# Performance work log

Measured on AMD Instinct MI355X. Metric: run time of the kernel, lower is better.

## Reference

```python
import math
import jax, jax.numpy as jnp
import numpy as np

B, N, D, H, HID = 2, 2048, 1024, 16, 4096
KS = (7, 25, 49)

def _alibi_slopes(n):
    def p2(m):
        start = 2.0 ** (-(2.0 ** (-(math.log2(m) - 3))))
        return [start * (start ** i) for i in range(m)]
    if math.log2(n).is_integer():
        s = p2(n)
    else:
        cp2 = 2 ** int(math.floor(math.log2(n)))
        s = p2(cp2) + p2(2 * cp2)[0::2][: n - cp2]
    return jnp.asarray(s, dtype=jnp.float32)

def _ln(x, g, b, eps=1e-5):
    m = x.mean(-1, keepdims=True)
    v = ((x - m) ** 2).mean(-1, keepdims=True)
    return (x - m) / jnp.sqrt(v + eps) * g + b

def _dwconv(x, w, pl, pr, mode, bias=None):
    # x: (B, D, L) channels-first, w: (D, 1, k) depthwise kernel
    xp = jnp.pad(x, ((0, 0), (0, 0), (pl, pr)), mode=mode)
    y = jax.lax.conv_general_dilated(xp, w, (1,), 'VALID',
                                     dimension_numbers=('NCH', 'OIH', 'NCH'),
                                     feature_group_count=x.shape[1])
    if bias is not None:
        y = y + bias[None, :, None]
    return y

def _forward(x, periodic_bias, alpha, dw7, dw25, dw49, ln1_g, ln1_b, ln2_g, ln2_b,
             Wq, bq, Wk, bk, Wv, bv, Wo, bo, W1, b1, W2, b2, tw, tb):
    Bx, Nx, Dm = x.shape
    hd = Dm // H
    # --- series decomposition: softmax-weighted multi-scale moving averages ---
    xt = x.transpose(0, 2, 1)  # (B, D, N)
    branches = [_dwconv(xt, w, k // 2, k // 2, 'reflect')
                for w, k in ((dw7, 7), (dw25, 25), (dw49, 49))]
    wmix = jax.nn.softmax(alpha)
    T = sum(br * wi for br, wi in zip(branches, wmix)).transpose(0, 2, 1)  # trend (B,N,D)
    S = x - T  # seasonal
    # --- ALiBi self-attention on normalized seasonal part ---
    sn = _ln(S, ln1_g, ln1_b)
    q = (jnp.einsum('bnd,ed->bne', sn, Wq) + bq).reshape(Bx, Nx, H, hd)
    k = (jnp.einsum('bnd,ed->bne', sn, Wk) + bk).reshape(Bx, Nx, H, hd)
    v = (jnp.einsum('bnd,ed->bne', sn, Wv) + bv).reshape(Bx, Nx, H, hd)
    logits = jnp.einsum('bqhd,bkhd->bhqk', q, k) / np.float32(np.sqrt(hd))
    idx = jnp.arange(Nx)
    dist = jnp.maximum(idx[None, :] - idx[:, None], 0).astype(jnp.float32)  # clamp(j-i, 0)
    slopes = _alibi_slopes(H)
    logits = logits - slopes[None, :, None, None] * dist[None, None] + periodic_bias[None, None]
    attn = jax.nn.softmax(logits, axis=-1)
    o = jnp.einsum('bhqk,bkhd->bqhd', attn, v).reshape(Bx, Nx, Dm)
    y = jnp.einsum('bnd,ed->bne', o, Wo) + bo
    x_s = S + y
    # --- dense FFN (exact GELU, as torch nn.GELU default) ---
    h = _ln(x_s, ln2_g, ln2_b)
    ffn = jnp.einsum('bnh,dh->bnd',
                     jax.nn.gelu(jnp.einsum('bnd,hd->bnh', h, W1) + b1, approximate=False),
                     W2) + b2
    x_s = x_s + ffn
    # --- trend path: depthwise conv k=5, zero padding 2 ---
    t_out = _dwconv(T.transpose(0, 2, 1), tw, 2, 2, 'constant', tb).transpose(0, 2, 1)
    return x_s + t_out

def setup_inputs():
    key = jax.random.key(0)
    ks = jax.random.split(key, 12)
    def lin(k, o, i):
        return jax.random.normal(k, (o, i), jnp.float32) / np.float32(np.sqrt(i))
    return {
        'x': jax.random.normal(ks[0], (B, N, D), jnp.float32),
        'periodic_bias': 0.1 * jax.random.normal(ks[1], (N, N), jnp.float32),
        'alpha': jnp.zeros((len(KS),), jnp.float32),
        'dw7': jnp.full((D, 1, 7), 1.0 / 7, jnp.float32),
        'dw25': jnp.full((D, 1, 25), 1.0 / 25, jnp.float32),
        'dw49': jnp.full((D, 1, 49), 1.0 / 49, jnp.float32),
        'ln1_g': jnp.ones((D,), jnp.float32), 'ln1_b': jnp.zeros((D,), jnp.float32),
        'ln2_g': jnp.ones((D,), jnp.float32), 'ln2_b': jnp.zeros((D,), jnp.float32),
        'Wq': lin(ks[2], D, D), 'bq': jnp.zeros((D,), jnp.float32),
        'Wk': lin(ks[3], D, D), 'bk': jnp.zeros((D,), jnp.float32),
        'Wv': lin(ks[4], D, D), 'bv': jnp.zeros((D,), jnp.float32),
        'Wo': lin(ks[5], D, D), 'bo': jnp.zeros((D,), jnp.float32),
        'W1': lin(ks[6], HID, D), 'b1': jnp.zeros((HID,), jnp.float32),
        'W2': lin(ks[7], D, HID), 'b2': jnp.zeros((D,), jnp.float32),
        'tw': 0.1 * jax.random.normal(ks[8], (D, 1, 5), jnp.float32),
        'tb': jnp.zeros((D,), jnp.float32),
    }

def reference(x, periodic_bias, alpha, dw7, dw25, dw49, ln1_g, ln1_b, ln2_g, ln2_b,
              Wq, bq, Wk, bk, Wv, bv, Wo, bo, W1, b1, W2, b2, tw, tb):
    out = _forward(x, periodic_bias, alpha, dw7, dw25, dw49, ln1_g, ln1_b, ln2_g, ln2_b,
                   Wq, bq, Wk, bk, Wv, bv, Wo, bo, W1, b1, W2, b2, tw, tb)
    return (out, jnp.zeros((), out.dtype))
```

## Files before the change

kernel.cpp:

```cpp
#include <hip/hip_runtime.h>
#include <cstdint>

#define BB 2
#define NN 2048
#define DD 1024
#define HH 16
#define HD 64
#define HID_ 4096
#define MM (BB*NN)

typedef __bf16 bf16x8 __attribute__((ext_vector_type(8)));
typedef float  f32x4  __attribute__((ext_vector_type(4)));

__device__ inline void gload_lds16(const void* g, void* l) {
  __builtin_amdgcn_global_load_lds((const __attribute__((address_space(1))) char*)g,
                                   (__attribute__((address_space(3))) char*)l, 16, 0, 0);
}

__global__ void k_wcomb(const float* __restrict__ alpha, const float* __restrict__ dw7,
                        const float* __restrict__ dw25, const float* __restrict__ dw49,
                        float* __restrict__ wc) {
  int t = blockIdx.x;
  float a0 = alpha[0], a1 = alpha[1], a2 = alpha[2];
  float mx = fmaxf(a0, fmaxf(a1, a2));
  float e0 = __expf(a0 - mx), e1 = __expf(a1 - mx), e2 = __expf(a2 - mx);
  float inv = 1.f / (e0 + e1 + e2);
  float w0 = e0 * inv, w1 = e1 * inv, w2 = e2 * inv;
  for (int d = threadIdx.x; d < DD; d += blockDim.x) {
    float v = w2 * dw49[d * 49 + t];
    if (t >= 12 && t <= 36) v += w1 * dw25[d * 25 + (t - 12)];
    if (t >= 21 && t <= 27) v += w0 * dw7[d * 7 + (t - 21)];
    wc[t * DD + d] = v;
  }
}

__global__ void k_bias3(const float* __restrict__ bq, const float* __restrict__ bk,
                        const float* __restrict__ bv, float* __restrict__ b3) {
  for (int i = threadIdx.x; i < 3 * DD; i += blockDim.x) {
    const float* s = (i < DD) ? bq : (i < 2 * DD ? bk : bv);
    b3[i] = s[i & (DD - 1)];
  }
}

__global__ __launch_bounds__(256) void k_cvtall(const float* __restrict__ Wq, const float* __restrict__ Wk,
                         const float* __restrict__ Wv, const float* __restrict__ Wo,
                         const float* __restrict__ W1, const float* __restrict__ W2,
                         __bf16* __restrict__ dst) {
  size_t i = ((size_t)blockIdx.x * 256 + threadIdx.x) * 4;
  const float* s;
  if (i < 1048576u) s = Wq + i;
  else if (i < 2097152u) s = Wk + (i - 1048576u);
  else if (i < 3145728u) s = Wv + (i - 2097152u);
  else if (i < 4194304u) s = Wo + (i - 3145728u);
  else if (i < 8388608u) s = W1 + (i - 4194304u);
  else s = W2 + (i - 8388608u);
  float4 v = *(const float4*)s;
  dst[i] = (__bf16)v.x; dst[i+1] = (__bf16)v.y; dst[i+2] = (__bf16)v.z; dst[i+3] = (__bf16)v.w;
}

__global__ __launch_bounds__(256) void k_pbt(const float* __restrict__ pb,
                                             __bf16* __restrict__ pbt) {
  int q = blockIdx.x;
  int qt16 = q >> 4, qm = q & 15;
  for (int k = threadIdx.x; k < NN; k += 256) {
    float v = pb[(size_t)q * NN + k] * 1.4426950408889634f;
    int kt = k >> 4, g = (k >> 2) & 3, rr = k & 3;
    pbt[((size_t)qt16 * 128 + kt) * 256 + (qm + 16 * g) * 4 + rr] = (__bf16)v;
  }
}

__global__ __launch_bounds__(256) void k_decomp(const float* __restrict__ x,
                                                const float* __restrict__ wc,
                                                float* __restrict__ T, float* __restrict__ S) {
  int bid = blockIdx.x;
  int db = bid & 3, ns = (bid >> 2) & 127, b = bid >> 9;
  int d = db * 256 + threadIdx.x;
  const float* xb = x + (size_t)b * NN * DD + d;
  float xw[64];
#pragma unroll
  for (int i = 0; i < 64; ++i) {
    int n = ns * 16 - 24 + i;
    n = (n < 0) ? -n : n;
    n = (n > NN - 1) ? 2 * (NN - 1) - n : n;
    xw[i] = xb[(size_t)n * DD];
  }
  float acc[16];
#pragma unroll
  for (int i = 0; i < 16; ++i) acc[i] = 0.f;
#pragma unroll
  for (int t = 0; t < 49; ++t) {
    float wv = wc[t * DD + d];
#pragma unroll
    for (int i = 0; i < 16; ++i) acc[i] = fmaf(wv, xw[i + t], acc[i]);
  }
  size_t base = ((size_t)b * NN + ns * 16) * DD + d;
#pragma unroll
  for (int i = 0; i < 16; ++i) {
    T[base + (size_t)i * DD] = acc[i];
    S[base + (size_t)i * DD] = xw[i + 24] - acc[i];
  }
}

__global__ __launch_bounds__(256) void k_tout(const float* __restrict__ T,
                                              const float* __restrict__ tw,
                                              const float* __restrict__ tb,
                                              float* __restrict__ tout) {
  int bid = blockIdx.x;
  int db = bid & 3, ns = (bid >> 2) & 127, b = bid >> 9;
  int d = db * 256 + threadIdx.x;
  const float* Tb = T + (size_t)b * NN * DD + d;
  float xw[20];
#pragma unroll
  for (int i = 0; i < 20; ++i) {
    int n = ns * 16 - 2 + i;
    xw[i] = (n < 0 || n >= NN) ? 0.f : Tb[(size_t)n * DD];
  }
  float bv = tb[d];
  float acc[16];
#pragma unroll
  for (int i = 0; i < 16; ++i) acc[i] = bv;
#pragma unroll
  for (int t = 0; t < 5; ++t) {
    float wv = tw[d * 5 + t];
#pragma unroll
    for (int i = 0; i < 16; ++i) acc[i] = fmaf(wv, xw[i + t], acc[i]);
  }
  size_t base = ((size_t)b * NN + ns * 16) * DD + d;
#pragma unroll
  for (int i = 0; i < 16; ++i) tout[base + (size_t)i * DD] = acc[i];
}

__global__ __launch_bounds__(256) void k_ln(const float* __restrict__ x,
                                            const float* __restrict__ g,
                                            const float* __restrict__ bt,
                                            __bf16* __restrict__ y) {
  int row = blockIdx.x;
  const float* xr = x + (size_t)row * DD;
  int i = threadIdx.x * 4;
  float4 v = *(const float4*)&xr[i];
  float s = v.x + v.y + v.z + v.w;
  float sq = v.x * v.x + v.y * v.y + v.z * v.z + v.w * v.w;
#pragma unroll
  for (int m = 1; m <= 32; m <<= 1) { s += __shfl_xor(s, m); sq += __shfl_xor(sq, m); }
  __shared__ float rs[4], rq[4];
  int wid = threadIdx.x >> 6;
  if ((threadIdx.x & 63) == 0) { rs[wid] = s; rq[wid] = sq; }
  __syncthreads();
  s = rs[0] + rs[1] + rs[2] + rs[3];
  sq = rq[0] + rq[1] + rq[2] + rq[3];
  float mean = s * (1.f / DD);
  float var = sq * (1.f / DD) - mean * mean;
  float rstd = rsqrtf(var + 1e-5f);
  float4 gv = *(const float4*)&g[i];
  float4 bv = *(const float4*)&bt[i];
  __bf16* yr = y + (size_t)row * DD + i;
  yr[0] = (__bf16)((v.x - mean) * rstd * gv.x + bv.x);
  yr[1] = (__bf16)((v.y - mean) * rstd * gv.y + bv.y);
  yr[2] = (__bf16)((v.z - mean) * rstd * gv.z + bv.z);
  yr[3] = (__bf16)((v.w - mean) * rstd * gv.w + bv.w);
}

template <int EPI, int BNT>
__global__ __launch_bounds__(256) void k_gemm(const __bf16* __restrict__ A,
                                              const __bf16* __restrict__ Bw, int K,
                                              const float* __restrict__ bias,
                                              const float* __restrict__ aux1,
                                              const float* __restrict__ aux2,
                                              float* __restrict__ outf,
                                              __bf16* __restrict__ outb) {
  constexpr int NFR = BNT / 32;
  __shared__ __bf16 aS[2][128 * 32];
  __shared__ __bf16 bS[2][BNT * 32];
  const int tid = threadIdx.x;
  const int lane = tid & 63;
  const int wid = tid >> 6;
  const int wm = wid >> 1, wn = wid & 1;
  const int r = lane & 15, gq = lane >> 4;
  const int m0 = blockIdx.y * 128;
  const int n0 = blockIdx.x * BNT;

  f32x4 acc[4][NFR];
#pragma unroll
  for (int mi = 0; mi < 4; ++mi)
#pragma unroll
    for (int ni = 0; ni < NFR; ++ni) acc[mi][ni] = (f32x4){0.f, 0.f, 0.f, 0.f};

  auto stage = [&](int bufi, int k0) {
#pragma unroll
    for (int i = 0; i < 2; ++i) {
      int e = i * 2048 + tid * 8;
      int row = e >> 5, col = e & 31;
      gload_lds16(A + (size_t)(m0 + row) * K + k0 + col, &aS[bufi][e]);
    }
#pragma unroll
    for (int i = 0; i < BNT / 64; ++i) {
      int e = i * 2048 + tid * 8;
      int row = e >> 5, col = e & 31;
      gload_lds16(Bw + (size_t)(n0 + row) * K + k0 + col, &bS[bufi][e]);
    }
  };

  stage(0, 0);
  const int nk = K >> 5;
  int buf = 0;
  for (int kt = 0; kt < nk; ++kt) {
    __syncthreads();
    if (kt + 1 < nk) stage(buf ^ 1, (kt + 1) << 5);
    bf16x8 af[4], bfr[NFR];
#pragma unroll
    for (int mi = 0; mi < 4; ++mi)
      af[mi] = *reinterpret_cast<const bf16x8*>(&aS[buf][(wm * 64 + mi * 16 + r) * 32 + gq * 8]);
#pragma unroll
    for (int ni = 0; ni < NFR; ++ni)
      bfr[ni] = *reinterpret_cast<const bf16x8*>(&bS[buf][(wn * (BNT / 2) + ni * 16 + r) * 32 + gq * 8]);
#pragma unroll
    for (int mi = 0; mi < 4; ++mi)
#pragma unroll
      for (int ni = 0; ni < NFR; ++ni)
        acc[mi][ni] = __builtin_amdgcn_mfma_f32_16x16x32_bf16(af[mi], bfr[ni], acc[mi][ni], 0, 0, 0);
    buf ^= 1;
  }

#pragma unroll
  for (int mi = 0; mi < 4; ++mi) {
#pragma unroll
    for (int ni = 0; ni < NFR; ++ni) {
      int colg = n0 + wn * (BNT / 2) + ni * 16 + r;
      float bcol = bias[colg];
#pragma unroll
      for (int rr = 0; rr < 4; ++rr) {
        int mg = m0 + wm * 64 + mi * 16 + gq * 4 + rr;
        float val = acc[mi][ni][rr] + bcol;
        if constexpr (EPI == 0) {
          int which = colg >> 10, e = colg & 1023;
          int hh = e >> 6, d = e & 63;
          int b = mg >> 11, nq = mg & (NN - 1);
          if (which == 2) {
            int nl = nq & 63, kk = nl & 31;
            int slot = ((kk >> 4) << 2) | (((kk >> 2) & 3) << 3) | (kk & 3) | (nl & 32);
            int nqp = (nq & ~63) | slot;
            outb[(size_t)2 * (BB * HH * NN * HD) +
                 ((size_t)((b * HH + hh) * HD + d)) * NN + nqp] = (__bf16)val;
          } else {
            outb[(size_t)which * (BB * HH * NN * HD) +
                 ((size_t)(b * HH + hh) * NN + nq) * HD + d] = (__bf16)val;
          }
        } else if constexpr (EPI == 1) {
          size_t idx = (size_t)mg * DD + colg;
          outf[idx] = aux1[idx] + val;
        } else if constexpr (EPI == 2) {
          float gl = val * 0.5f * (1.f + erff(val * 0.70710678118f));
          outb[(size_t)mg * HID_ + colg] = (__bf16)gl;
        } else {
          size_t idx = (size_t)mg * DD + colg;
          outf[idx] = val + aux1[idx] + aux2[idx];
        }
      }
    }
  }
}

__global__ __launch_bounds__(512) void k_attn(const __bf16* __restrict__ qb,
                                              const __bf16* __restrict__ kb,
                                              const __bf16* __restrict__ vtb,
                                              const __bf16* __restrict__ pbt,
                                              __bf16* __restrict__ ob) {
  __shared__ __bf16 kS[2][64 * 64];
  __shared__ __bf16 vS[2][64 * 64];
  int blk = blockIdx.x;
  int qt = blk & 15, bh = blk >> 4;
  int h = bh & (HH - 1), b = bh >> 4;
  int tid = threadIdx.x;
  int lane = tid & 63, w = tid >> 6;
  int r = lane & 15, g = lane >> 4;
  const __bf16* Kp = kb + (size_t)bh * NN * HD;
  const __bf16* Vt = vtb + (size_t)bh * HD * NN;
  int qbase = qt * 128 + w * 16;
  int cq = qt * 2 + (w >> 2);
  const __bf16* Q = qb + ((size_t)bh * NN + qbase) * HD;

  bf16x8 qf0 = *(const bf16x8*)&Q[(size_t)r * HD + g * 8];
  bf16x8 qf1 = *(const bf16x8*)&Q[(size_t)r * HD + 32 + g * 8];
  bf16x8 onesf;
#pragma unroll
  for (int j = 0; j < 8; ++j) onesf[j] = (__bf16)1.0f;

  const float C = 0.18033688011112042f;
  const float THRL2 = 11.541560327111707f;
  float slope = exp2f(-0.5f * (float)(h + 1)) * 1.4426950408889634f;
  float sconst[16];
#pragma unroll
  for (int st = 0; st < 4; ++st)
#pragma unroll
    for (int rr = 0; rr < 4; ++rr) sconst[st * 4 + rr] = slope * (float)(st * 16 + rr);
  float aL = slope * (float)(g * 4 - r);

  float m = 0.f;
  f32x4 oacc[4], lacc;
#pragma unroll
  for (int t = 0; t < 4; ++t) oacc[t] = (f32x4){0.f, 0.f, 0.f, 0.f};
  lacc = (f32x4){0.f, 0.f, 0.f, 0.f};

  auto stage = [&](int bufi, int kc0) {
    int row = tid >> 3;
    int c = (tid & 7) * 8;
    int src = c ^ ((row & 7) * 8);
    gload_lds16(Kp + (size_t)(kc0 + row) * HD + src, &kS[bufi][tid * 8]);
    gload_lds16(Vt + (size_t)row * NN + kc0 + src, &vS[bufi][tid * 8]);
  };

  stage(0, 0);
  int buf = 0;
  size_t tilebase = (size_t)(qt * 8 + w) * 128;
  int sw = (r & 7) * 8;

  for (int ch = 0; ch < NN / 64; ++ch) {
    int kc0 = ch * 64;
    __syncthreads();
    if (ch + 1 < NN / 64) stage(buf ^ 1, kc0 + 64);

    uint2 ub[4];
#pragma unroll
    for (int st = 0; st < 4; ++st)
      ub[st] = *(const uint2*)&pbt[(tilebase + (kc0 >> 4) + st) * 256 + lane * 4];

    f32x4 sacc[4];
#pragma unroll
    for (int st = 0; st < 4; ++st) {
      sacc[st] = (f32x4){0.f, 0.f, 0.f, 0.f};
      int rowb = (st * 16 + r) * 64;
      bf16x8 kf0 = *(const bf16x8*)&kS[buf][rowb + ((g * 8) ^ sw)];
      bf16x8 kf1 = *(const bf16x8*)&kS[buf][rowb + ((32 + g * 8) ^ sw)];
      sacc[st] = __builtin_amdgcn_mfma_f32_16x16x32_bf16(kf0, qf0, sacc[st], 0, 0, 0);
      sacc[st] = __builtin_amdgcn_mfma_f32_16x16x32_bf16(kf1, qf1, sacc[st], 0, 0, 0);
    }

    float zm[16];
    if (ch > cq) {
      float uu = fmaf(slope, (float)(kc0 - qbase), aL) + m;
#pragma unroll
      for (int st = 0; st < 4; ++st) {
        float p0 = __uint_as_float(ub[st].x << 16);
        float p1 = __uint_as_float(ub[st].x & 0xffff0000u);
        float p2 = __uint_as_float(ub[st].y << 16);
        float p3 = __uint_as_float(ub[st].y & 0xffff0000u);
        zm[st*4+0] = fmaf(sacc[st][0], C, p0) - uu - sconst[st*4+0];
        zm[st*4+1] = fmaf(sacc[st][1], C, p1) - uu - sconst[st*4+1];
        zm[st*4+2] = fmaf(sacc[st][2], C, p2) - uu - sconst[st*4+2];
        zm[st*4+3] = fmaf(sacc[st][3], C, p3) - uu - sconst[st*4+3];
      }
    } else if (ch < cq) {
#pragma unroll
      for (int st = 0; st < 4; ++st) {
        float p0 = __uint_as_float(ub[st].x << 16);
        float p1 = __uint_as_float(ub[st].x & 0xffff0000u);
        float p2 = __uint_as_float(ub[st].y << 16);
        float p3 = __uint_as_float(ub[st].y & 0xffff0000u);
        zm[st*4+0] = fmaf(sacc[st][0], C, p0) - m;
        zm[st*4+1] = fmaf(sacc[st][1], C, p1) - m;
        zm[st*4+2] = fmaf(sacc[st][2], C, p2) - m;
        zm[st*4+3] = fmaf(sacc[st][3], C, p3) - m;
      }
    } else {
      int kqb = kc0 + g * 4 - qbase - r;
#pragma unroll
      for (int st = 0; st < 4; ++st) {
        float p0 = __uint_as_float(ub[st].x << 16);
        float p1 = __uint_as_float(ub[st].x & 0xffff0000u);
        float p2 = __uint_as_float(ub[st].y << 16);
        float p3 = __uint_as_float(ub[st].y & 0xffff0000u);
        float pb4[4] = {p0, p1, p2, p3};
#pragma unroll
        for (int rr = 0; rr < 4; ++rr) {
          int dk = kqb + st * 16 + rr;
          float dist = (dk > 0) ? (float)dk : 0.f;
          zm[st*4+rr] = fmaf(sacc[st][rr], C, pb4[rr]) - fmaf(slope, dist, m);
        }
      }
    }

    float zmax = zm[0];
#pragma unroll
    for (int j = 1; j < 16; ++j) zmax = fmaxf(zmax, zm[j]);
    if (__any(zmax > THRL2)) {
      float rowmax = fmaxf(zmax, __shfl_xor(zmax, 16));
      rowmax = fmaxf(rowmax, __shfl_xor(rowmax, 32));
      float delta = fmaxf(rowmax, 0.f);
      m += delta;
      float sc = exp2f(-delta);
      float sco[4];
#pragma unroll
      for (int rr = 0; rr < 4; ++rr) sco[rr] = __shfl(sc, g * 4 + rr);
#pragma unroll
      for (int rr = 0; rr < 4; ++rr) {
        lacc[rr] *= sco[rr];
#pragma unroll
        for (int t = 0; t < 4; ++t) oacc[t][rr] *= sco[rr];
      }
#pragma unroll
      for (int j = 0; j < 16; ++j) zm[j] -= delta;
    }

    bf16x8 pa0, pa1;
#pragma unroll
    for (int j = 0; j < 8; ++j) {
      pa0[j] = (__bf16)exp2f(zm[(j >> 2) * 4 + (j & 3)]);
      pa1[j] = (__bf16)exp2f(zm[(2 + (j >> 2)) * 4 + (j & 3)]);
    }

#pragma unroll
    for (int t = 0; t < 4; ++t) {
      int rowb = (t * 16 + r) * 64;
      bf16x8 vf0 = *(const bf16x8*)&vS[buf][rowb + ((g * 8) ^ sw)];
      bf16x8 vf1 = *(const bf16x8*)&vS[buf][rowb + ((32 + g * 8) ^ sw)];
      oacc[t] = __builtin_amdgcn_mfma_f32_16x16x32_bf16(pa0, vf0, oacc[t], 0, 0, 0);
      oacc[t] = __builtin_amdgcn_mfma_f32_16x16x32_bf16(pa1, vf1, oacc[t], 0, 0, 0);
    }
    lacc = __builtin_amdgcn_mfma_f32_16x16x32_bf16(pa0, onesf, lacc, 0, 0, 0);
    lacc = __builtin_amdgcn_mfma_f32_16x16x32_bf16(pa1, onesf, lacc, 0, 0, 0);
    buf ^= 1;
  }

#pragma unroll
  for (int rr = 0; rr < 4; ++rr) {
    int qg = qbase + g * 4 + rr;
    float inv = 1.f / lacc[rr];
#pragma unroll
    for (int t = 0; t < 4; ++t) {
      float v = oacc[t][rr] * inv;
      ob[((size_t)(b * NN) + qg) * DD + h * HD + t * 16 + r] = (__bf16)v;
    }
  }
}

__global__ void k_tail(float* __restrict__ out) { out[(size_t)BB * NN * DD] = 0.f; }

extern "C" void kernel_launch(void* const* d_in, const int* in_sizes, int n_in,
                              void* d_out, int out_size, void* d_ws, size_t ws_size,
                              hipStream_t stream) {
  const float* x    = (const float*)d_in[0];
  const float* pb   = (const float*)d_in[1];
  const float* alpha= (const float*)d_in[2];
  const float* dw7  = (const float*)d_in[3];
  const float* dw25 = (const float*)d_in[4];
  const float* dw49 = (const float*)d_in[5];
  const float* ln1g = (const float*)d_in[6];
  const float* ln1b = (const float*)d_in[7];
  const float* ln2g = (const float*)d_in[8];
  const float* ln2b = (const float*)d_in[9];
  const float* Wq   = (const float*)d_in[10];
  const float* bq   = (const float*)d_in[11];
  const float* Wk   = (const float*)d_in[12];
  const float* bk   = (const float*)d_in[13];
  const float* Wv   = (const float*)d_in[14];
  const float* bv   = (const float*)d_in[15];
  const float* Wo   = (const float*)d_in[16];
  const float* bo   = (const float*)d_in[17];
  const float* W1   = (const float*)d_in[18];
  const float* b1   = (const float*)d_in[19];
  const float* W2   = (const float*)d_in[20];
  const float* b2   = (const float*)d_in[21];
  const float* tw   = (const float*)d_in[22];
  const float* tb   = (const float*)d_in[23];
  float* out = (float*)d_out;

  char* w = (char*)d_ws;
  size_t off = 0;
  auto alloc = [&](size_t bytes) -> char* {
    char* p = w + off;
    off = (off + bytes + 255) & ~(size_t)255;
    return p;
  };
  float*  wc    = (float*)alloc(49 * 1024 * 4);
  float*  b3    = (float*)alloc(3072 * 4);
  float*  Tbuf  = (float*)alloc((size_t)MM * DD * 4);
  float*  Sbuf  = (float*)alloc((size_t)MM * DD * 4);
  float*  toutb = (float*)alloc((size_t)MM * DD * 4);
  __bf16* sn    = (__bf16*)alloc((size_t)MM * DD * 2);
  __bf16* qkv   = (__bf16*)alloc((size_t)3 * MM * DD * 2);
  __bf16* gb    = (__bf16*)alloc((size_t)MM * HID_ * 2);
  __bf16* wall  = (__bf16*)alloc((size_t)12582912 * 2);
  __bf16* pbt   = (__bf16*)alloc((size_t)NN * NN * 2);
  __bf16* wqkvb = wall;
  __bf16* wob   = wall + (size_t)3 * DD * DD;
  __bf16* w1b   = wall + (size_t)4 * DD * DD;
  __bf16* w2b   = wall + (size_t)4 * DD * DD + (size_t)HID_ * DD;
  float*  xs    = Tbuf;
  __bf16* obuf  = sn;
  __bf16* hb    = qkv;

  const size_t BHND = (size_t)BB * HH * NN * HD;

  k_wcomb<<<49, 256, 0, stream>>>(alpha, dw7, dw25, dw49, wc);
  k_bias3<<<1, 256, 0, stream>>>(bq, bk, bv, b3);
  k_pbt<<<NN, 256, 0, stream>>>(pb, pbt);
  k_cvtall<<<12288, 256, 0, stream>>>(Wq, Wk, Wv, Wo, W1, W2, wall);
  k_decomp<<<1024, 256, 0, stream>>>(x, wc, Tbuf, Sbuf);
  k_tout<<<1024, 256, 0, stream>>>(Tbuf, tw, tb, toutb);
  k_ln<<<MM, 256, 0, stream>>>(Sbuf, ln1g, ln1b, sn);
  k_gemm<0,128><<<dim3(24, 32), 256, 0, stream>>>(sn, wqkvb, DD, b3, nullptr, nullptr, nullptr, qkv);
  k_attn<<<BB * HH * (NN / 128), 512, 0, stream>>>(qkv, qkv + BHND, qkv + 2 * BHND, pbt, obuf);
  k_gemm<1,64><<<dim3(16, 32), 256, 0, stream>>>(obuf, wob, DD, bo, Sbuf, nullptr, xs, nullptr);
  k_ln<<<MM, 256, 0, stream>>>(xs, ln2g, ln2b, hb);
  k_gemm<2,128><<<dim3(32, 32), 256, 0, stream>>>(hb, w1b, DD, b1, nullptr, nullptr, nullptr, gb);
  k_gemm<3,64><<<dim3(16, 32), 256, 0, stream>>>(gb, w2b, HID_, b2, xs, toutb, out, nullptr);
  k_tail<<<1, 1, 0, stream>>>(out);
}
```

Measured before the change: 353.6 us.

## Fuse trend conv into decomp, deepen GEMM K-tile with swizzle, tune attention scheduling

Merges the trend-output depthwise conv into the decomposition kernel by computing 20 trend rows per thread, which removes the T buffer round trip and one launch. The GEMM gains a K-tile template parameter; three of the four GEMMs now use 64-wide K tiles with an XOR-swizzled LDS layout, halving the barrier count. MFMA sections in the GEMM and attention are wrapped in s_setprio. Attention blocks are remapped across the grid and the row max uses 3-input max. These are several independent tweaks that cost extra LDS and registers, which may lower occupancy.

```diff
diff --git a/kernel.cpp b/kernel.cpp
--- a/kernel.cpp
+++ b/kernel.cpp
@@ -16,6 +16,7 @@
   __builtin_amdgcn_global_load_lds((const __attribute__((address_space(1))) char*)g,
                                    (__attribute__((address_space(3))) char*)l, 16, 0, 0);
 }
+__device__ inline float max3f(float a, float b, float c) { return fmaxf(fmaxf(a, b), c); }
 
 __global__ void k_wcomb(const float* __restrict__ alpha, const float* __restrict__ dw7,
                         const float* __restrict__ dw25, const float* __restrict__ dw49,
@@ -71,63 +72,50 @@
 
 __global__ __launch_bounds__(256) void k_decomp(const float* __restrict__ x,
                                                 const float* __restrict__ wc,
-                                                float* __restrict__ T, float* __restrict__ S) {
+                                                const float* __restrict__ tw,
+                                                const float* __restrict__ tb,
+                                                float* __restrict__ S,
+                                                float* __restrict__ tout) {
   int bid = blockIdx.x;
   int db = bid & 3, ns = (bid >> 2) & 127, b = bid >> 9;
   int d = db * 256 + threadIdx.x;
+  int n0 = ns * 16;
   const float* xb = x + (size_t)b * NN * DD + d;
-  float xw[64];
-#pragma unroll
-  for (int i = 0; i < 64; ++i) {
-    int n = ns * 16 - 24 + i;
+  float xw[68];
+#pragma unroll
+  for (int i = 0; i < 68; ++i) {
+    int n = n0 - 26 + i;
     n = (n < 0) ? -n : n;
     n = (n > NN - 1) ? 2 * (NN - 1) - n : n;
     xw[i] = xb[(size_t)n * DD];
   }
-  float acc[16];
-#pragma unroll
-  for (int i = 0; i < 16; ++i) acc[i] = 0.f;
+  float Tx[20];
+#pragma unroll
+  for (int j = 0; j < 20; ++j) Tx[j] = 0.f;
 #pragma unroll
   for (int t = 0; t < 49; ++t) {
     float wv = wc[t * DD + d];
 #pragma unroll
-    for (int i = 0; i < 16; ++i) acc[i] = fmaf(wv, xw[i + t], acc[i]);
-  }
-  size_t base = ((size_t)b * NN + ns * 16) * DD + d;
+    for (int j = 0; j < 20; ++j) Tx[j] = fmaf(wv, xw[j + t], Tx[j]);
+  }
+#pragma unroll
+  for (int j = 0; j < 20; ++j) {
+    int row = n0 - 2 + j;
+    if (row < 0 || row >= NN) Tx[j] = 0.f;
+  }
+  float tw5[5];
+#pragma unroll
+  for (int t = 0; t < 5; ++t) tw5[t] = tw[d * 5 + t];
+  float tbv = tb[d];
+  size_t base = ((size_t)b * NN + n0) * DD + d;
 #pragma unroll
   for (int i = 0; i < 16; ++i) {
-    T[base + (size_t)i * DD] = acc[i];
-    S[base + (size_t)i * DD] = xw[i + 24] - acc[i];
-  }
-}
-
-__global__ __launch_bounds__(256) void k_tout(const float* __restrict__ T,
-                                              const float* __restrict__ tw,
-                                              const float* __restrict__ tb,
-                                              float* __restrict__ tout) {
-  int bid = blockIdx.x;
-  int db = bid & 3, ns = (bid >> 2) & 127, b = bid >> 9;
-  int d = db * 256 + threadIdx.x;
-  const float* Tb = T + (size_t)b * NN * DD + d;
-  float xw[20];
-#pragma unroll
-  for (int i = 0; i < 20; ++i) {
-    int n = ns * 16 - 2 + i;
-    xw[i] = (n < 0 || n >= NN) ? 0.f : Tb[(size_t)n * DD];
-  }
-  float bv = tb[d];
-  float acc[16];
-#pragma unroll
-  for (int i = 0; i < 16; ++i) acc[i] = bv;
-#pragma unroll
-  for (int t = 0; t < 5; ++t) {
-    float wv = tw[d * 5 + t];
-#pragma unroll
-    for (int i = 0; i < 16; ++i) acc[i] = fmaf(wv, xw[i + t], acc[i]);
-  }
-  size_t base = ((size_t)b * NN + ns * 16) * DD + d;
-#pragma unroll
-  for (int i = 0; i < 16; ++i) tout[base + (size_t)i * DD] = acc[i];
+    S[base + (size_t)i * DD] = xw[i + 26] - Tx[i + 2];
+    float acc = tbv;
+#pragma unroll
+    for (int t = 0; t < 5; ++t) acc = fmaf(tw5[t], Tx[i + t], acc);
+    tout[base + (size_t)i * DD] = acc;
+  }
 }
 
 __global__ __launch_bounds__(256) void k_ln(const float* __restrict__ x,
@@ -160,7 +148,7 @@
   yr[3] = (__bf16)((v.w - mean) * rstd * gv.w + bv.w);
 }
 
-template <int EPI, int BNT>
+template <int EPI, int BNT, int BKT>
 __global__ __launch_bounds__(256) void k_gemm(const __bf16* __restrict__ A,
                                               const __bf16* __restrict__ Bw, int K,
                                               const float* __restrict__ bias,
@@ -169,8 +157,9 @@
                                               float* __restrict__ outf,
                                               __bf16* __restrict__ outb) {
   constexpr int NFR = BNT / 32;
-  __shared__ __bf16 aS[2][128 * 32];
-  __shared__ __bf16 bS[2][BNT * 32];
+  constexpr int NKK = BKT / 32;
+  __shared__ __bf16 aS[2][128 * BKT];
+  __shared__ __bf16 bS[2][BNT * BKT];
   const int tid = threadIdx.x;
   const int lane = tid & 63;
   const int wid = tid >> 6;
@@ -178,6 +167,7 @@
   const int r = lane & 15, gq = lane >> 4;
   const int m0 = blockIdx.y * 128;
   const int n0 = blockIdx.x * BNT;
+  const int rsw = (BKT == 64) ? (r & 7) * 8 : 0;
 
   f32x4 acc[4][NFR];
 #pragma unroll
@@ -187,37 +177,49 @@
 
   auto stage = [&](int bufi, int k0) {
 #pragma unroll
-    for (int i = 0; i < 2; ++i) {
+    for (int i = 0; i < (128 * BKT) / 2048; ++i) {
       int e = i * 2048 + tid * 8;
-      int row = e >> 5, col = e & 31;
-      gload_lds16(A + (size_t)(m0 + row) * K + k0 + col, &aS[bufi][e]);
-    }
-#pragma unroll
-    for (int i = 0; i < BNT / 64; ++i) {
+      int row = e / BKT, col = e % BKT;
+      int src = (BKT == 64) ? (col ^ ((row & 7) * 8)) : col;
+      gload_lds16(A + (size_t)(m0 + row) * K + k0 + src, &aS[bufi][e]);
+    }
+#pragma unroll
+    for (int i = 0; i < (BNT * BKT) / 2048; ++i) {
       int e = i * 2048 + tid * 8;
-      int row = e >> 5, col = e & 31;
-      gload_lds16(Bw + (size_t)(n0 + row) * K + k0 + col, &bS[bufi][e]);
+      int row = e / BKT, col = e % BKT;
+      int src = (BKT == 64) ? (col ^ ((row & 7) * 8)) : col;
+      gload_lds16(Bw + (size_t)(n0 + row) * K + k0 + src, &bS[bufi][e]);
     }
   };
 
   stage(0, 0);
-  const int nk = K >> 5;
+  const int nk = K / BKT;
   int buf = 0;
   for (int kt = 0; kt < nk; ++kt) {
     __syncthreads();
-    if (kt + 1 < nk) stage(buf ^ 1, (kt + 1) << 5);
-    bf16x8 af[4], bfr[NFR];
+    if (kt + 1 < nk) stage(buf ^ 1, (kt + 1) * BKT);
+    bf16x8 af[4][NKK], bfr[NFR][NKK];
 #pragma unroll
     for (int mi = 0; mi < 4; ++mi)
-      af[mi] = *reinterpret_cast<const bf16x8*>(&aS[buf][(wm * 64 + mi * 16 + r) * 32 + gq * 8]);
+#pragma unroll
+      for (int kk = 0; kk < NKK; ++kk)
+        af[mi][kk] = *reinterpret_cast<const bf16x8*>(
+            &aS[buf][(wm * 64 + mi * 16 + r) * BKT + ((kk * 32 + gq * 8) ^ rsw)]);
 #pragma unroll
     for (int ni = 0; ni < NFR; ++ni)
-      bfr[ni] = *reinterpret_cast<const bf16x8*>(&bS[buf][(wn * (BNT / 2) + ni * 16 + r) * 32 + gq * 8]);
-#pragma unroll
-    for (int mi = 0; mi < 4; ++mi)
-#pragma unroll
-      for (int ni = 0; ni < NFR; ++ni)
-        acc[mi][ni] = __builtin_amdgcn_mfma_f32_16x16x32_bf16(af[mi], bfr[ni], acc[mi][ni], 0, 0, 0);
+#pragma unroll
+      for (int kk = 0; kk < NKK; ++kk)
+        bfr[ni][kk] = *reinterpret_cast<const bf16x8*>(
+            &bS[buf][(wn * (BNT / 2) + ni * 16 + r) * BKT + ((kk * 32 + gq * 8) ^ rsw)]);
+    __builtin_amdgcn_s_setprio(1);
+#pragma unroll
+    for (int kk = 0; kk < NKK; ++kk)
+#pragma unroll
+      for (int mi = 0; mi < 4; ++mi)
+#pragma unroll
+        for (int ni = 0; ni < NFR; ++ni)
+          acc[mi][ni] = __builtin_amdgcn_mfma_f32_16x16x32_bf16(af[mi][kk], bfr[ni][kk], acc[mi][ni], 0, 0, 0);
+    __builtin_amdgcn_s_setprio(0);
     buf ^= 1;
   }
 
@@ -267,7 +269,7 @@
                                               __bf16* __restrict__ ob) {
   __shared__ __bf16 kS[2][64 * 64];
   __shared__ __bf16 vS[2][64 * 64];
-  int blk = blockIdx.x;
+  int blk = ((blockIdx.x & 7) << 6) | (blockIdx.x >> 3);
   int qt = blk & 15, bh = blk >> 4;
   int h = bh & (HH - 1), b = bh >> 4;
   int tid = threadIdx.x;
@@ -325,6 +327,7 @@
       ub[st] = *(const uint2*)&pbt[(tilebase + (kc0 >> 4) + st) * 256 + lane * 4];
 
     f32x4 sacc[4];
+    __builtin_amdgcn_s_setprio(1);
 #pragma unroll
     for (int st = 0; st < 4; ++st) {
       sacc[st] = (f32x4){0.f, 0.f, 0.f, 0.f};
@@ -334,6 +337,7 @@
       sacc[st] = __builtin_amdgcn_mfma_f32_16x16x32_bf16(kf0, qf0, sacc[st], 0, 0, 0);
       sacc[st] = __builtin_amdgcn_mfma_f32_16x16x32_bf16(kf1, qf1, sacc[st], 0, 0, 0);
     }
+    __builtin_amdgcn_s_setprio(0);
 
     float zm[16];
     if (ch > cq) {
@@ -379,9 +383,12 @@
       }
     }
 
-    float zmax = zm[0];
-#pragma unroll
-    for (int j = 1; j < 16; ++j) zmax = fmaxf(zmax, zm[j]);
+    float l0 = max3f(zm[0], zm[1], zm[2]);
+    float l1 = max3f(zm[3], zm[4], zm[5]);
+    float l2 = max3f(zm[6], zm[7], zm[8]);
+    float l3 = max3f(zm[9], zm[10], zm[11]);
+    float l4 = max3f(zm[12], zm[13], zm[14]);
+    float zmax = fmaxf(max3f(l0, l1, l2), max3f(l3, l4, zm[15]));
     if (__any(zmax > THRL2)) {
       float rowmax = fmaxf(zmax, __shfl_xor(zmax, 16));
       rowmax = fmaxf(rowmax, __shfl_xor(rowmax, 32));
@@ -408,6 +415,7 @@
       pa1[j] = (__bf16)exp2f(zm[(2 + (j >> 2)) * 4 + (j & 3)]);
     }
 
+    __builtin_amdgcn_s_setprio(1);
 #pragma unroll
     for (int t = 0; t < 4; ++t) {
       int rowb = (t * 16 + r) * 64;
@@ -418,6 +426,7 @@
     }
     lacc = __builtin_amdgcn_mfma_f32_16x16x32_bf16(pa0, onesf, lacc, 0, 0, 0);
     lacc = __builtin_amdgcn_mfma_f32_16x16x32_bf16(pa1, onesf, lacc, 0, 0, 0);
+    __builtin_amdgcn_s_setprio(0);
     buf ^= 1;
   }
 
@@ -495,14 +504,13 @@
   k_bias3<<<1, 256, 0, stream>>>(bq, bk, bv, b3);
   k_pbt<<<NN, 256, 0, stream>>>(pb, pbt);
   k_cvtall<<<12288, 256, 0, stream>>>(Wq, Wk, Wv, Wo, W1, W2, wall);
-  k_decomp<<<1024, 256, 0, stream>>>(x, wc, Tbuf, Sbuf);
-  k_tout<<<1024, 256, 0, stream>>>(Tbuf, tw, tb, toutb);
+  k_decomp<<<1024, 256, 0, stream>>>(x, wc, tw, tb, Sbuf, toutb);
   k_ln<<<MM, 256, 0, stream>>>(Sbuf, ln1g, ln1b, sn);
-  k_gemm<0,128><<<dim3(24, 32), 256, 0, stream>>>(sn, wqkvb, DD, b3, nullptr, nullptr, nullptr, qkv);
+  k_gemm<0,128,32><<<dim3(24, 32), 256, 0, stream>>>(sn, wqkvb, DD, b3, nullptr, nullptr, nullptr, qkv);
   k_attn<<<BB * HH * (NN / 128), 512, 0, stream>>>(qkv, qkv + BHND, qkv + 2 * BHND, pbt, obuf);
-  k_gemm<1,64><<<dim3(16, 32), 256, 0, stream>>>(obuf, wob, DD, bo, Sbuf, nullptr, xs, nullptr);
+  k_gemm<1,64,64><<<dim3(16, 32), 256, 0, stream>>>(obuf, wob, DD, bo, Sbuf, nullptr, xs, nullptr);
   k_ln<<<MM, 256, 0, stream>>>(xs, ln2g, ln2b, hb);
-  k_gemm<2,128><<<dim3(32, 32), 256, 0, stream>>>(hb, w1b, DD, b1, nullptr, nullptr, nullptr, gb);
-  k_gemm<3,64><<<dim3(16, 32), 256, 0, stream>>>(gb, w2b, HID_, b2, xs, toutb, out, nullptr);
+  k_gemm<2,128,64><<<dim3(32, 32), 256, 0, stream>>>(hb, w1b, DD, b1, nullptr, nullptr, nullptr, gb);
+  k_gemm<3,64,64><<<dim3(16, 32), 256, 0, stream>>>(gb, w2b, HID_, b2, xs, toutb, out, nullptr);
   k_tail<<<1, 1, 0, stream>>>(out);
 }
```

Measured after the change: 325.5 us. -8.0%, faster.
